# Optimization experiments

Measured on AMD Instinct MI355X. Metric: run time of the kernel, lower is better.

The kernel has to match this reference:

```python
import math
import jax, jax.numpy as jnp
import numpy as np

B, T, C, H = 4, 2048, 1024, 16
D = C // H  # head dim = 64


def setup_inputs() -> dict:
    key = jax.random.key(0)
    ks = jax.random.split(key, 5)
    s = 1.0 / math.sqrt(C)
    return {
        "x": jax.random.normal(ks[0], (B, T, C), jnp.float32),
        "w_qkv": jax.random.normal(ks[1], (C, 3 * C), jnp.float32) * s,
        "b_qkv": jax.random.normal(ks[2], (3 * C,), jnp.float32) * 0.02,
        "w_out": jax.random.normal(ks[3], (C, C), jnp.float32) * s,
        "b_out": jax.random.normal(ks[4], (C,), jnp.float32) * 0.02,
    }


def reference(x, w_qkv, b_qkv, w_out, b_out):
    # qkv projection: (B,T,C) @ (C,3C) -> split into Q,K,V
    qkv = x @ w_qkv + b_qkv
    q, k, v = jnp.split(qkv, 3, axis=-1)
    # reshape to (B,H,T,D)
    q = q.reshape(B, T, H, D).transpose(0, 2, 1, 3)
    k = k.reshape(B, T, H, D).transpose(0, 2, 1, 3)
    v = v.reshape(B, T, H, D).transpose(0, 2, 1, 3)
    # scaled scores with causal mask
    scores = jnp.einsum("bhqd,bhkd->bhqk", q, k) * (1.0 / math.sqrt(D))
    causal = jnp.tril(jnp.ones((T, T), dtype=bool))
    scores = jnp.where(causal[None, None], scores, -jnp.inf)
    attn = jax.nn.softmax(scores, axis=-1)  # dropout_rate=0 (eval)
    out = jnp.einsum("bhqk,bhkd->bhqd", attn, v)
    out = out.transpose(0, 2, 1, 3).reshape(B, T, C)
    return out @ w_out + b_out
```

## Files before the change

### kernel.cpp

```cpp
#include <hip/hip_runtime.h>
#include <cstdint>
#include <cstddef>

typedef _Float16 h8_t __attribute__((ext_vector_type(8)));
typedef _Float16 h4_t __attribute__((ext_vector_type(4)));
typedef float f32x4 __attribute__((ext_vector_type(4)));
typedef float f32x16 __attribute__((ext_vector_type(16)));
typedef unsigned u32x4 __attribute__((ext_vector_type(4)));

#define MFMA_16x16x32_F16(a, b, c) __builtin_amdgcn_mfma_f32_16x16x32_f16(a, b, c, 0, 0, 0)
#define MFMA_32x32x16_F16(a, b, c) __builtin_amdgcn_mfma_f32_32x32x16_f16(a, b, c, 0, 0, 0)

__device__ inline void gload_lds16(const void* g, void* l) {
  __builtin_amdgcn_global_load_lds((const __attribute__((address_space(1))) void*)g,
                                   (__attribute__((address_space(3))) void*)l, 16, 0, 0);
}

__global__ void cvt_f16_kernel(const float* __restrict__ in, _Float16* __restrict__ out, int n4) {
  int i = blockIdx.x * 256 + threadIdx.x;
  if (i >= n4) return;
  float4 v = reinterpret_cast<const float4*>(in)[i];
  h4_t h;
  h[0] = (_Float16)v.x; h[1] = (_Float16)v.y; h[2] = (_Float16)v.z; h[3] = (_Float16)v.w;
  reinterpret_cast<h4_t*>(out)[i] = h;
}

__global__ void transpose_cvt_kernel(const float* __restrict__ in, _Float16* __restrict__ out,
                                     int R, int Cc) {
  __shared__ float tile[32][33];
  int tx = threadIdx.x & 31;
  int ty = threadIdx.x >> 5;
  int c0 = blockIdx.x * 32;
  int r0 = blockIdx.y * 32;
#pragma unroll
  for (int i = 0; i < 4; ++i)
    tile[ty + i * 8][tx] = in[(size_t)(r0 + ty + i * 8) * Cc + (c0 + tx)];
  __syncthreads();
#pragma unroll
  for (int i = 0; i < 4; ++i)
    out[(size_t)(c0 + ty + i * 8) * R + (r0 + tx)] = (_Float16)tile[tx][ty + i * 8];
}

template <int EPI>
__global__ __launch_bounds__(256, 2) void gemm_bt_kernel(
    const _Float16* __restrict__ A, const _Float16* __restrict__ Bt,
    const float* __restrict__ bias, _Float16* __restrict__ outQ,
    _Float16* __restrict__ outK, _Float16* __restrict__ outV,
    float* __restrict__ outF, int NB) {
  __shared__ _Float16 Al[2][4096];
  __shared__ _Float16 Bl[2][4096];
  const int tid = threadIdx.x;
  const int lane = tid & 63;
  const int w = tid >> 6;
  const int bm = blockIdx.x / NB;
  const int bn = blockIdx.x % NB;
  const int wm = w & 1, wn = w >> 1;
  const int m0 = bm * 128, n0 = bn * 128;

  f32x4 acc[4][4];
#pragma unroll
  for (int m = 0; m < 4; ++m)
#pragma unroll
    for (int n = 0; n < 4; ++n) acc[m][n] = (f32x4){0.f, 0.f, 0.f, 0.f};

  auto stage = [&](int buf, int kt) {
    const int k0 = kt * 32;
#pragma unroll
    for (int c = 0; c < 2; ++c) {
      const int seg = w * 2 + c;
      const int row = seg * 16 + (lane >> 2);
      const int chunk = (lane & 3) ^ ((row >> 1) & 3);
      gload_lds16(&A[(size_t)(m0 + row) * 1024 + k0 + chunk * 8], &Al[buf][seg * 512 + lane * 8]);
      gload_lds16(&Bt[(size_t)(n0 + row) * 1024 + k0 + chunk * 8], &Bl[buf][seg * 512 + lane * 8]);
    }
  };

  stage(0, 0);
  __syncthreads();

#pragma unroll 1
  for (int t = 0; t < 32; ++t) {
    const int buf = t & 1;
    if (t + 1 < 32) stage(buf ^ 1, t + 1);
    h8_t af[4], bf[4];
#pragma unroll
    for (int i = 0; i < 4; ++i) {
      const int row = wm * 64 + i * 16 + (lane & 15);
      af[i] = *(const h8_t*)&Al[buf][row * 32 + (((lane >> 4) ^ ((row >> 1) & 3)) * 8)];
    }
#pragma unroll
    for (int j = 0; j < 4; ++j) {
      const int row = wn * 64 + j * 16 + (lane & 15);
      bf[j] = *(const h8_t*)&Bl[buf][row * 32 + (((lane >> 4) ^ ((row >> 1) & 3)) * 8)];
    }
#pragma unroll
    for (int i = 0; i < 4; ++i)
#pragma unroll
      for (int j = 0; j < 4; ++j)
        acc[i][j] = MFMA_16x16x32_F16(af[i], bf[j], acc[i][j]);
    __syncthreads();
  }

  const int gm0 = bm * 128 + wm * 64;
  const int gn0 = bn * 128 + wn * 64;
#pragma unroll
  for (int i = 0; i < 4; ++i) {
#pragma unroll
    for (int j = 0; j < 4; ++j) {
      const int gn = gn0 + j * 16 + (lane & 15);
      const int tm0 = gm0 + i * 16 + (lane >> 4) * 4;
      const float bv = bias[gn];
      if (EPI == 0) {
        const int which = gn >> 10;
        const int nn = gn & 1023;
        const int h = nn >> 6, d = nn & 63;
        const int t0 = tm0 & 2047, b = tm0 >> 11;
        const int bh = b * 16 + h;
        if (which == 2) {
          h4_t pack;
#pragma unroll
          for (int r = 0; r < 4; ++r) pack[r] = (_Float16)(acc[i][j][r] + bv);
          *reinterpret_cast<h4_t*>(&outV[((size_t)bh * 64 + d) * 2048 + t0]) = pack;
        } else {
          _Float16* dst = (which == 0) ? outQ : outK;
          const float scale = (which == 0) ? 0.18033688011112042f : 1.0f;
#pragma unroll
          for (int r = 0; r < 4; ++r)
            dst[((size_t)bh * 2048 + t0 + r) * 64 + d] = (_Float16)((acc[i][j][r] + bv) * scale);
        }
      } else {
#pragma unroll
        for (int r = 0; r < 4; ++r)
          outF[(size_t)(tm0 + r) * 1024 + gn] = acc[i][j][r] + bv;
      }
    }
  }
}

__device__ inline void stage_kv(const _Float16* __restrict__ Kbh, const _Float16* __restrict__ Vbh,
                                int kt, _Float16* Kd, _Float16* Vd, int w, int lane) {
  const _Float16* Kg = Kbh + (size_t)kt * 64 * 64;
  const _Float16* Vg = Vbh + kt * 64;
#pragma unroll
  for (int c = 0; c < 2; ++c) {
    const int idx = (2 * w + c) * 64 + lane;
    const int row = idx >> 3;
    const int chs = (idx & 7) ^ (row & 7);
    gload_lds16(Kg + row * 64 + chs * 8, Kd + idx * 8);
    gload_lds16(Vg + (size_t)row * 2048 + chs * 8, Vd + idx * 8);
  }
}

__device__ inline void pack_pfrag(const float* e, h8_t* out) {
  unsigned u[8];
#pragma unroll
  for (int i = 0; i < 8; ++i) {
    auto hv = __builtin_amdgcn_cvt_pkrtz(e[2 * i], e[2 * i + 1]);
    u[i] = __builtin_bit_cast(unsigned, hv);
  }
  auto r02 = __builtin_amdgcn_permlane32_swap(u[0], u[2], false, false);
  auto r13 = __builtin_amdgcn_permlane32_swap(u[1], u[3], false, false);
  auto r46 = __builtin_amdgcn_permlane32_swap(u[4], u[6], false, false);
  auto r57 = __builtin_amdgcn_permlane32_swap(u[5], u[7], false, false);
  u32x4 w0 = {(unsigned)r02[0], (unsigned)r13[0], (unsigned)r02[1], (unsigned)r13[1]};
  u32x4 w1 = {(unsigned)r46[0], (unsigned)r57[0], (unsigned)r46[1], (unsigned)r57[1]};
  out[0] = __builtin_bit_cast(h8_t, w0);
  out[1] = __builtin_bit_cast(h8_t, w1);
}

__global__ __launch_bounds__(256, 2) void attn_kernel(
    const _Float16* __restrict__ Q, const _Float16* __restrict__ K,
    const _Float16* __restrict__ Vt, _Float16* __restrict__ O) {
  __shared__ _Float16 Kl[2][64 * 64];
  __shared__ _Float16 Vl[2][64 * 64];
  const int tid = threadIdx.x;
  const int lane = tid & 63;
  const int w = tid >> 6;
  const int hi = lane >> 5;
  const int l31 = lane & 31;
  const int bh = blockIdx.x >> 3;
  const int pr = blockIdx.x & 7;
  const int b = bh >> 4, h = bh & 15;
  const _Float16* Kbh = K + (size_t)bh * 2048 * 64;
  const _Float16* Vbh = Vt + (size_t)bh * 64 * 2048;

#pragma unroll
  for (int gi = 0; gi < 2; ++gi) {
    const int g = gi ? (15 - pr) : pr;
    const int nt = 2 * g + 2;
    const int qbase = g * 128 + w * 32;
    const int qrow = qbase + l31;

    h8_t qf[4];
    const _Float16* Qp = Q + ((size_t)bh * 2048 + qrow) * 64 + hi * 8;
#pragma unroll
    for (int ds = 0; ds < 4; ++ds)
      qf[ds] = *reinterpret_cast<const h8_t*>(Qp + ds * 16);

    f32x16 oa[2] = {};
    float m = -1e30f, lsum = 0.f;

    stage_kv(Kbh, Vbh, 0, &Kl[0][0], &Vl[0][0], w, lane);
    __syncthreads();

    for (int kt = 0; kt < nt; ++kt) {
      const int cur = kt & 1;
      if (kt + 1 < nt)
        stage_kv(Kbh, Vbh, kt + 1, &Kl[cur ^ 1][0], &Vl[cur ^ 1][0], w, lane);

      if (kt * 64 <= qbase + 31) {
        const char* Kb = (const char*)&Kl[cur][0];
        const char* Vb = (const char*)&Vl[cur][0];
        f32x16 s0 = {}, s1 = {};
#pragma unroll
        for (int ds = 0; ds < 4; ++ds) {
          const int bc = ds * 32 + hi * 16;
          h8_t kf0 = *(const h8_t*)(Kb + l31 * 128 + (bc ^ ((l31 & 7) << 4)));
          h8_t kf1 = *(const h8_t*)(Kb + (32 + l31) * 128 + (bc ^ ((l31 & 7) << 4)));
          s0 = MFMA_32x32x16_F16(kf0, qf[ds], s0);
          s1 = MFMA_32x32x16_F16(kf1, qf[ds], s1);
        }
        if (kt >= 2 * g) {
#pragma unroll
          for (int r = 0; r < 16; ++r) {
            const int kr = kt * 64 + (r & 3) + 8 * (r >> 2) + 4 * hi;
            if (kr > qrow) s0[r] = -1e30f;
            if (kr + 32 > qrow) s1[r] = -1e30f;
          }
        }
        float t[16];
#pragma unroll
        for (int r = 0; r < 16; ++r) t[r] = fmaxf(s0[r], s1[r]);
#pragma unroll
        for (int st = 8; st >= 1; st >>= 1)
#pragma unroll
          for (int r = 0; r < st; ++r) t[r] = fmaxf(t[r], t[r + st]);
        const float pmax = fmaxf(t[0], __shfl_xor(t[0], 32));
        const float mnew = fmaxf(m, pmax);
        if (__any(mnew > m + 8.f)) {
          const float al = __builtin_amdgcn_exp2f(m - mnew);
          lsum *= al;
#pragma unroll
          for (int r = 0; r < 16; ++r) { oa[0][r] *= al; oa[1][r] *= al; }
          m = mnew;
        }
        float e0[16], e1[16];
#pragma unroll
        for (int r = 0; r < 16; ++r) {
          e0[r] = __builtin_amdgcn_exp2f(s0[r] - m);
          e1[r] = __builtin_amdgcn_exp2f(s1[r] - m);
        }
        float ps = 0.f;
#pragma unroll
        for (int r = 0; r < 16; ++r) ps += e0[r] + e1[r];
        ps += __shfl_xor(ps, 32);
        lsum += ps;
        h8_t pf[4];
        pack_pfrag(e0, pf + 0);
        pack_pfrag(e1, pf + 2);
#pragma unroll
        for (int dt = 0; dt < 2; ++dt) {
#pragma unroll
          for (int kg = 0; kg < 4; ++kg) {
            const int row = dt * 32 + l31;
            const int bc = kg * 32 + hi * 16;
            h8_t vf = *(const h8_t*)(Vb + row * 128 + (bc ^ ((row & 7) << 4)));
            oa[dt] = MFMA_32x32x16_F16(vf, pf[kg], oa[dt]);
          }
        }
      }
      __syncthreads();
    }

    const float inv = __builtin_amdgcn_rcpf(lsum);
    _Float16* Op = O + ((size_t)b * 2048 + qrow) * 1024 + h * 64;
#pragma unroll
    for (int dt = 0; dt < 2; ++dt) {
#pragma unroll
      for (int rg = 0; rg < 4; ++rg) {
        h4_t pk4;
#pragma unroll
        for (int i = 0; i < 4; ++i) pk4[i] = (_Float16)(oa[dt][rg * 4 + i] * inv);
        *reinterpret_cast<h4_t*>(Op + dt * 32 + rg * 8 + hi * 4) = pk4;
      }
    }
  }
}

extern "C" void kernel_launch(void* const* d_in, const int* in_sizes, int n_in,
                              void* d_out, int out_size, void* d_ws, size_t ws_size,
                              hipStream_t stream) {
  (void)in_sizes; (void)n_in; (void)out_size; (void)ws_size;
  const float* x = (const float*)d_in[0];
  const float* w_qkv = (const float*)d_in[1];
  const float* b_qkv = (const float*)d_in[2];
  const float* w_out = (const float*)d_in[3];
  const float* b_out = (const float*)d_in[4];
  float* out = (float*)d_out;

  char* ws = (char*)d_ws;
  size_t off = 0;
  auto alloc = [&](size_t bytes) {
    void* p = ws + off;
    off += (bytes + 255) & ~(size_t)255;
    return p;
  };
  _Float16* x16 = (_Float16*)alloc((size_t)8192 * 1024 * 2);
  _Float16* wqkvT = (_Float16*)alloc((size_t)3072 * 1024 * 2);
  _Float16* woutT = (_Float16*)alloc((size_t)1024 * 1024 * 2);
  _Float16* Qh = (_Float16*)alloc((size_t)64 * 2048 * 64 * 2);
  _Float16* Kh = (_Float16*)alloc((size_t)64 * 2048 * 64 * 2);
  _Float16* Vth = (_Float16*)alloc((size_t)64 * 64 * 2048 * 2);
  _Float16* Oh = (_Float16*)alloc((size_t)8192 * 1024 * 2);

  cvt_f16_kernel<<<8192, 256, 0, stream>>>(x, x16, 8192 * 1024 / 4);
  transpose_cvt_kernel<<<dim3(3072 / 32, 1024 / 32), 256, 0, stream>>>(w_qkv, wqkvT, 1024, 3072);
  transpose_cvt_kernel<<<dim3(1024 / 32, 1024 / 32), 256, 0, stream>>>(w_out, woutT, 1024, 1024);
  gemm_bt_kernel<0><<<64 * 24, 256, 0, stream>>>(x16, wqkvT, b_qkv, Qh, Kh, Vth, nullptr, 24);
  attn_kernel<<<64 * 8, 256, 0, stream>>>(Qh, Kh, Vth, Oh);
  gemm_bt_kernel<1><<<64 * 8, 256, 0, stream>>>(Oh, woutT, b_out, nullptr, nullptr, nullptr, out, 8);
}
```

Baseline: 185.7 us.

## Triple-buffer GEMM LDS staging with manual vmcnt waits and raw barriers

Converts the projection GEMM's double-buffered LDS pipeline to a three-stage pipeline that prefetches two K-tiles ahead. It replaces __syncthreads with explicit s_waitcnt vmcnt(4) plus a raw s_barrier, so the one newer tile's loads can stay in flight across the barrier. It also precomputes global and LDS address offsets outside the loop and raises launch_bounds occupancy to 3 blocks. The cost is more LDS (48KB per block) and more register pressure, and it relies on hand-counted vmcnt being correct.

```diff
diff --git a/kernel.cpp b/kernel.cpp
--- a/kernel.cpp
+++ b/kernel.cpp
@@ -15,6 +15,9 @@
   __builtin_amdgcn_global_load_lds((const __attribute__((address_space(1))) void*)g,
                                    (__attribute__((address_space(3))) void*)l, 16, 0, 0);
 }
+
+#define CFENCE asm volatile("" ::: "memory")
+#define RAW_BAR() do { CFENCE; __builtin_amdgcn_s_barrier(); CFENCE; } while (0)
 
 __global__ void cvt_f16_kernel(const float* __restrict__ in, _Float16* __restrict__ out, int n4) {
   int i = blockIdx.x * 256 + threadIdx.x;
@@ -42,13 +45,13 @@
 }
 
 template <int EPI>
-__global__ __launch_bounds__(256, 2) void gemm_bt_kernel(
+__global__ __launch_bounds__(256, 3) void gemm_bt_kernel(
     const _Float16* __restrict__ A, const _Float16* __restrict__ Bt,
     const float* __restrict__ bias, _Float16* __restrict__ outQ,
     _Float16* __restrict__ outK, _Float16* __restrict__ outV,
     float* __restrict__ outF, int NB) {
-  __shared__ _Float16 Al[2][4096];
-  __shared__ _Float16 Bl[2][4096];
+  __shared__ _Float16 Al[3][4096];
+  __shared__ _Float16 Bl[3][4096];
   const int tid = threadIdx.x;
   const int lane = tid & 63;
   const int w = tid >> 6;
@@ -63,42 +66,63 @@
 #pragma unroll
     for (int n = 0; n < 4; ++n) acc[m][n] = (f32x4){0.f, 0.f, 0.f, 0.f};
 
+  const int seg0 = w * 2, seg1 = w * 2 + 1;
+  const int r0s = seg0 * 16 + (lane >> 2);
+  const int r1s = seg1 * 16 + (lane >> 2);
+  const int c0s = ((lane & 3) ^ ((r0s >> 1) & 3)) * 8;
+  const int c1s = ((lane & 3) ^ ((r1s >> 1) & 3)) * 8;
+  const _Float16* aS0 = A + (size_t)(m0 + r0s) * 1024 + c0s;
+  const _Float16* aS1 = A + (size_t)(m0 + r1s) * 1024 + c1s;
+  const _Float16* bS0 = Bt + (size_t)(n0 + r0s) * 1024 + c0s;
+  const _Float16* bS1 = Bt + (size_t)(n0 + r1s) * 1024 + c1s;
+  const int d0 = seg0 * 512 + lane * 8;
+  const int d1 = seg1 * 512 + lane * 8;
+
   auto stage = [&](int buf, int kt) {
     const int k0 = kt * 32;
-#pragma unroll
-    for (int c = 0; c < 2; ++c) {
-      const int seg = w * 2 + c;
-      const int row = seg * 16 + (lane >> 2);
-      const int chunk = (lane & 3) ^ ((row >> 1) & 3);
-      gload_lds16(&A[(size_t)(m0 + row) * 1024 + k0 + chunk * 8], &Al[buf][seg * 512 + lane * 8]);
-      gload_lds16(&Bt[(size_t)(n0 + row) * 1024 + k0 + chunk * 8], &Bl[buf][seg * 512 + lane * 8]);
-    }
+    gload_lds16(aS0 + k0, &Al[buf][d0]);
+    gload_lds16(bS0 + k0, &Bl[buf][d0]);
+    gload_lds16(aS1 + k0, &Al[buf][d1]);
+    gload_lds16(bS1 + k0, &Bl[buf][d1]);
   };
 
+  int offA[4], offB[4];
+#pragma unroll
+  for (int i = 0; i < 4; ++i) {
+    const int rowA = wm * 64 + i * 16 + (lane & 15);
+    offA[i] = rowA * 32 + (((lane >> 4) ^ ((rowA >> 1) & 3)) * 8);
+    const int rowB = wn * 64 + i * 16 + (lane & 15);
+    offB[i] = rowB * 32 + (((lane >> 4) ^ ((rowB >> 1) & 3)) * 8);
+  }
+
   stage(0, 0);
-  __syncthreads();
-
+  stage(1, 1);
+  asm volatile("s_waitcnt vmcnt(4)" ::: "memory");
+  RAW_BAR();
+
+  int cur = 0;
 #pragma unroll 1
   for (int t = 0; t < 32; ++t) {
-    const int buf = t & 1;
-    if (t + 1 < 32) stage(buf ^ 1, t + 1);
+    int nb = cur + 2; if (nb >= 3) nb -= 3;
+    if (t + 2 < 32) stage(nb, t + 2);
+    const _Float16* Ab = &Al[cur][0];
+    const _Float16* Bb = &Bl[cur][0];
     h8_t af[4], bf[4];
 #pragma unroll
-    for (int i = 0; i < 4; ++i) {
-      const int row = wm * 64 + i * 16 + (lane & 15);
-      af[i] = *(const h8_t*)&Al[buf][row * 32 + (((lane >> 4) ^ ((row >> 1) & 3)) * 8)];
-    }
-#pragma unroll
-    for (int j = 0; j < 4; ++j) {
-      const int row = wn * 64 + j * 16 + (lane & 15);
-      bf[j] = *(const h8_t*)&Bl[buf][row * 32 + (((lane >> 4) ^ ((row >> 1) & 3)) * 8)];
-    }
+    for (int i = 0; i < 4; ++i) af[i] = *(const h8_t*)&Ab[offA[i]];
+#pragma unroll
+    for (int j = 0; j < 4; ++j) bf[j] = *(const h8_t*)&Bb[offB[j]];
 #pragma unroll
     for (int i = 0; i < 4; ++i)
 #pragma unroll
       for (int j = 0; j < 4; ++j)
         acc[i][j] = MFMA_16x16x32_F16(af[i], bf[j], acc[i][j]);
-    __syncthreads();
+    if (t < 31) {
+      if (t + 2 < 32) asm volatile("s_waitcnt vmcnt(4)" ::: "memory");
+      else asm volatile("s_waitcnt vmcnt(0)" ::: "memory");
+      RAW_BAR();
+    }
+    ++cur; if (cur == 3) cur = 0;
   }
 
   const int gm0 = bm * 128 + wm * 64;
```

Result: no change. 184.2 us (-0.8%).
